# Kernel optimization log

Hardware: AMD Instinct MI355X
Metric: run time of the kernel (lower is better)

## Reference

```python
import jax, jax.numpy as jnp
import numpy as np

B, S, NC, ND, V = 16, 512, 10000, 10000, 128


def _rn(k, shape, scale=0.05):
    return jax.random.normal(k, shape, dtype=jnp.float32) * scale


def setup_inputs() -> dict:
    key = jax.random.key(0)
    ks = jax.random.split(key, 24)
    inp = {
        'c_seq': jax.random.randint(ks[0], (B, S), 0, NC),
        'd_seq': jax.random.randint(ks[1], (B, S), 0, ND),
        'r_seq': jax.random.uniform(ks[2], (B, S), dtype=jnp.float32),
        # embeddings / vectors
        'D1_w': _rn(ks[3], (ND, 1)),
        'D2_w': _rn(ks[4], (ND, V)),
        'v_r': _rn(ks[5], (V,)),
        'v_beta': _rn(ks[6], (V,)),
        # GRU (torch layout: gates ordered r,z,n; W_ih [3V,2V], W_hh [3V,V])
        'W_ih': _rn(ks[7], (3 * V, 2 * V)),
        'W_hh': _rn(ks[8], (3 * V, V)),
        'b_ih': jnp.zeros((3 * V,), jnp.float32),
        'b_hh': jnp.zeros((3 * V,), jnp.float32),
        # linear_1: V -> V -> V -> 1 (weights stored [in, out])
        'm1_W1': _rn(ks[9], (V, V)), 'm1_b1': jnp.zeros((V,), jnp.float32),
        'm1_W2': _rn(ks[10], (V, V)), 'm1_b2': jnp.zeros((V,), jnp.float32),
        'm1_W3': _rn(ks[11], (V, 1)), 'm1_b3': jnp.zeros((1,), jnp.float32),
        # linear_2: 3V -> V -> V -> 1
        'm2_W1': _rn(ks[12], (3 * V, V)), 'm2_b1': jnp.zeros((V,), jnp.float32),
        'm2_W2': _rn(ks[13], (V, V)), 'm2_b2': jnp.zeros((V,), jnp.float32),
        'm2_W3': _rn(ks[14], (V, 1)), 'm2_b3': jnp.zeros((1,), jnp.float32),
    }
    return inp


def _mlp(x, W1, b1, W2, b2, W3, b3):
    h = jax.nn.relu(x @ W1 + b1)
    h = jax.nn.relu(h @ W2 + b2)
    return h @ W3 + b3


def _gru_seq(x, W_ih, W_hh, b_ih, b_hh):
    # x: [B,S,2V] -> h_seq [B,S,V]; torch GRU gate order r,z,n
    xp = x @ W_ih.T + b_ih  # [B,S,3V]

    def step(h, xt):
        hp = h @ W_hh.T + b_hh
        xr, xz, xn = jnp.split(xt, 3, axis=-1)
        hr, hz, hn = jnp.split(hp, 3, axis=-1)
        r = jax.nn.sigmoid(xr + hr)
        z = jax.nn.sigmoid(xz + hz)
        n = jnp.tanh(xn + r * hn)
        h_new = (1.0 - z) * n + z * h
        return h_new, h_new

    h0 = jnp.zeros((x.shape[0], W_hh.shape[1]), x.dtype)
    _, hs = jax.lax.scan(step, h0, jnp.swapaxes(xp, 0, 1))  # [S,B,V]
    return jnp.swapaxes(hs, 0, 1)


def reference(c_seq, d_seq, r_seq, D1_w, D2_w, v_r, v_beta,
              W_ih, W_hh, b_ih, b_hh,
              m1_W1, m1_b1, m1_W2, m1_b2, m1_W3, m1_b3,
              m2_W1, m2_b1, m2_W2, m2_b2, m2_W3, m2_b3):
    v_d_seq = D2_w[d_seq]                     # [B,S,V]
    v_r_seq = r_seq[..., None] * v_r          # [B,S,V]

    h_seq = _gru_seq(jnp.concatenate([v_d_seq, v_r_seq], axis=-1),
                     W_ih, W_hh, b_ih, b_hh)  # [B,S,V]
    alpha_seq = _mlp(h_seq, m1_W1, m1_b1, m1_W2, m1_b2, m1_W3, m1_b3)[..., 0]  # [B,S]

    bidx = jnp.arange(c_seq.shape[0])

    def step(C, ins):
        c_t, vd_t, vr_t = ins                 # [B], [B,V], [B,V]
        beta_prev = C[bidx, c_t]              # gather: [B]
        v_beta_prev = beta_prev[:, None] * v_beta  # [B,V]
        new_c = _mlp(jnp.concatenate([v_beta_prev, vd_t, vr_t], axis=-1),
                     m2_W1, m2_b1, m2_W2, m2_b2, m2_W3, m2_b3)[:, 0]  # [B]
        C = C.at[bidx, c_t].set(new_c)        # scatter
        return C, (C, new_c)

    C0 = jnp.zeros((c_seq.shape[0], NC), jnp.float32)
    _, (C_seq, beta_seq) = jax.lax.scan(
        step, C0,
        (jnp.swapaxes(c_seq, 0, 1), jnp.swapaxes(v_d_seq, 0, 1), jnp.swapaxes(v_r_seq, 0, 1)))
    C_seq = jnp.swapaxes(C_seq, 0, 1)[..., None]   # [B,S,NC,1]
    beta_seq = jnp.swapaxes(beta_seq, 0, 1)        # [B,S]

    gamma_seq = D1_w[d_seq][..., 0]                # [B,S]
    return (alpha_seq, beta_seq, gamma_seq, h_seq, C_seq)
```

## Files before the change

kernel.cpp:

```cpp
#include <hip/hip_runtime.h>

#define Bq   16
#define Sq   512
#define Vq   128
#define NCq  10000

typedef __attribute__((ext_vector_type(8))) short short8v;
typedef __attribute__((ext_vector_type(4))) float f32x4;

#define OFF_XP     0u
#define OFF_PRE1   3145728u
#define OFF_WTIH   4194304u
#define OFF_WVRIH  4243456u
#define OFF_WVR1   4243840u
#define OFF_WVB    4243968u
#define OFF_PO     4244096u

__device__ __forceinline__ unsigned short f2bf(float x) {
    unsigned u = __builtin_bit_cast(unsigned, x);
    unsigned r = (u + 0x7fffu + ((u >> 16) & 1u)) >> 16;
    return (unsigned short)r;
}

__global__ __launch_bounds__(256) void k0_prep(
    const int* __restrict__ c_seq, const int* __restrict__ d_seq,
    const float* __restrict__ D1_w,
    const float* __restrict__ W_ih,
    const float* __restrict__ v_r, const float* __restrict__ v_beta,
    const float* __restrict__ m2W1,
    float* __restrict__ ws, float* __restrict__ gamma_out)
{
    const int blk = blockIdx.x, tid = threadIdx.x;

    if (blk < 128) {
        float* WTIH = ws + OFF_WTIH;
        int base = blk * 384;
        for (int i = tid; i < 384; i += 256) {
            int e = base + i;
            int k = e / 384, g = e % 384;
            WTIH[e] = W_ih[g * 256 + k];
        }
    } else if (blk == 128) {
        float* WVRIH = ws + OFF_WVRIH;
        float* WVR1  = ws + OFF_WVR1;
        float* WVB   = ws + OFF_WVB;
        for (int g = tid; g < 384; g += 256) {
            float a = 0.f;
            for (int k = 0; k < 128; ++k) a = fmaf(v_r[k], W_ih[g * 256 + 128 + k], a);
            WVRIH[g] = a;
        }
        if (tid < 128) {
            float a = 0.f, b = 0.f;
            for (int k = 0; k < 128; ++k) {
                a = fmaf(v_r[k],    m2W1[(256 + k) * 128 + tid], a);
                b = fmaf(v_beta[k], m2W1[k * 128 + tid],         b);
            }
            WVR1[tid] = a; WVB[tid] = b;
        }
    } else if (blk < 145) {
        const int b = blk - 129;
        __shared__ int cs[Sq];
        for (int i = tid; i < Sq; i += 256) cs[i] = c_seq[b * Sq + i];
        __syncthreads();
        int* PO = (int*)(ws + OFF_PO);
        for (int t = tid; t < Sq; t += 256) {
            int c = cs[t];
            int po = -1;
            for (int u = t - 1; u >= 0; --u) if (cs[u] == c) { po = u; break; }
            PO[t * 16 + b] = po;
        }
    } else {
        const int b = blk - 145;
        for (int s = tid; s < Sq; s += 256)
            gamma_out[b * Sq + s] = D1_w[d_seq[b * Sq + s]];
    }
}

__global__ __launch_bounds__(256) void k1_gemm(
    const int* __restrict__ d_seq, const float* __restrict__ D2_w,
    const float* __restrict__ m2W1,
    const float* __restrict__ b_ih, const float* __restrict__ b_hh,
    const float* __restrict__ r_seq, const float* __restrict__ m2b1,
    float* __restrict__ ws)
{
    __shared__ float As[64 * 128];
    __shared__ float Bs[128 * 64];
    const int blk = blockIdx.x, tid = threadIdx.x;
    const int nc = blk & 7;
    const int m0 = (blk >> 3) * 64;
    const float* WTIH = ws + OFF_WTIH;

    const float4* D2v = (const float4*)D2_w;
    for (int e = tid; e < 2048; e += 256) {
        int r = e >> 5, q = e & 31;
        int d = d_seq[m0 + r];
        *(float4*)&As[r * 128 + 4 * q] = D2v[d * 32 + q];
    }
    for (int e = tid; e < 2048; e += 256) {
        int k = e >> 4, q = e & 15;
        float4 v;
        if (nc < 6) v = *(const float4*)&WTIH[k * 384 + nc * 64 + 4 * q];
        else        v = *(const float4*)&m2W1[(128 + k) * 128 + (nc - 6) * 64 + 4 * q];
        *(float4*)&Bs[k * 64 + 4 * q] = v;
    }
    __syncthreads();

    const int tx = tid & 15, ty = tid >> 4;
    const int c0 = 4 * tx, r0 = 4 * ty;
    float acc[4][4];
#pragma unroll
    for (int i = 0; i < 4; ++i)
#pragma unroll
        for (int j = 0; j < 4; ++j) acc[i][j] = 0.f;

    for (int k = 0; k < 128; ++k) {
        float4 bv = *(const float4*)&Bs[k * 64 + c0];
#pragma unroll
        for (int i = 0; i < 4; ++i) {
            float a = As[(r0 + i) * 128 + k];
            acc[i][0] = fmaf(a, bv.x, acc[i][0]);
            acc[i][1] = fmaf(a, bv.y, acc[i][1]);
            acc[i][2] = fmaf(a, bv.z, acc[i][2]);
            acc[i][3] = fmaf(a, bv.w, acc[i][3]);
        }
    }

    float rsv[4];
#pragma unroll
    for (int i = 0; i < 4; ++i) rsv[i] = r_seq[m0 + r0 + i];

    if (nc < 6) {
        const int grow0 = nc * 64 + c0;
        float4 bi  = *(const float4*)&b_ih[grow0];
        float4 wv4 = *(const float4*)&(ws + OFF_WVRIH)[grow0];
        float4 bh4 = make_float4(0.f, 0.f, 0.f, 0.f);
        if (nc < 4) bh4 = *(const float4*)&b_hh[grow0];
        float* XP4 = ws + OFF_XP;
        const int r4 = grow0 >> 2;
#pragma unroll
        for (int i = 0; i < 4; ++i) {
            int row = m0 + r0 + i;
            int t = row & 511, bb = row >> 9;
            float4 v;
            v.x = acc[i][0] + bi.x + bh4.x + rsv[i] * wv4.x;
            v.y = acc[i][1] + bi.y + bh4.y + rsv[i] * wv4.y;
            v.z = acc[i][2] + bi.z + bh4.z + rsv[i] * wv4.z;
            v.w = acc[i][3] + bi.w + bh4.w + rsv[i] * wv4.w;
            *(float4*)&XP4[((t * 96 + r4) * 16 + bb) * 4] = v;
        }
    } else {
        const int j0 = (nc - 6) * 64 + c0;
        float4 b1v = *(const float4*)&m2b1[j0];
        float4 wr1 = *(const float4*)&(ws + OFF_WVR1)[j0];
        float* PRE1 = ws + OFF_PRE1;
#pragma unroll
        for (int i = 0; i < 4; ++i) {
            int row = m0 + r0 + i;
            float4 v;
            v.x = acc[i][0] + b1v.x + rsv[i] * wr1.x;
            v.y = acc[i][1] + b1v.y + rsv[i] * wr1.y;
            v.z = acc[i][2] + b1v.z + rsv[i] * wr1.z;
            v.w = acc[i][3] + b1v.w + rsv[i] * wr1.w;
            *(float4*)&PRE1[(size_t)row * 128 + j0] = v;
        }
    }
}

#define PLN 136
#define PLSZ (16*PLN+8)

__global__ __launch_bounds__(512, 1) void k2_scan(
    const float* __restrict__ W_hh, const float* __restrict__ b_hh,
    const float* __restrict__ m2W2, const float* __restrict__ m2b2,
    const float* __restrict__ m2W3, const float* __restrict__ m2b3,
    float* __restrict__ ws,
    float* __restrict__ hseq_out, float* __restrict__ beta_out)
{
    __shared__ __align__(16) unsigned char smem[70416];
    const int tid = threadIdx.x;
    const int l = tid & 63, wv = tid >> 6;
    const int qq = l >> 4, cb = l & 15;

    if (blockIdx.x == 0) {
        unsigned short* hP = (unsigned short*)smem;
        short8v aH[3][4];
#pragma unroll
        for (int g = 0; g < 3; ++g) {
            const float* wrow = W_hh + (g * 128 + 16 * wv + cb) * 128;
#pragma unroll
            for (int kf = 0; kf < 4; ++kf) {
                short8v hi;
#pragma unroll
                for (int e = 0; e < 8; ++e) hi[e] = (short)f2bf(wrow[kf * 32 + qq * 8 + e]);
                aH[g][kf] = hi;
            }
        }
        float bhn[4];
        *(float4*)bhn = *(const float4*)&b_hh[256 + 16 * wv + 4 * qq];
        const float* XP4 = ws + OFF_XP;

        f32x4 pxA[3], pxB[3], pxC[3];
#pragma unroll
        for (int g = 0; g < 3; ++g) {
            const int r4 = 32 * g + 4 * wv + qq;
            pxA[g] = *(const f32x4*)&XP4[((0 * 96 + r4) * 16 + cb) * 4];
            pxB[g] = *(const f32x4*)&XP4[((1 * 96 + r4) * 16 + cb) * 4];
            pxC[g] = (f32x4){0.f, 0.f, 0.f, 0.f};
        }
        float hold[4] = {0.f, 0.f, 0.f, 0.f};
        for (int i = tid; i < 2 * PLSZ; i += 512) hP[i] = 0;
        __syncthreads();

        for (int t = 0; t < 512; ++t) {
            const unsigned short* HI = hP + (t & 1) * PLSZ;
            unsigned short* HIn = hP + ((t + 1) & 1) * PLSZ;
            if (t < 510) {
#pragma unroll
                for (int g = 0; g < 3; ++g) {
                    const int r4 = 32 * g + 4 * wv + qq;
                    pxC[g] = *(const f32x4*)&XP4[(((t + 2) * 96 + r4) * 16 + cb) * 4];
                }
            }
            f32x4 C0 = {0.f,0.f,0.f,0.f}, C1 = {0.f,0.f,0.f,0.f}, C2 = {0.f,0.f,0.f,0.f};
#pragma unroll
            for (int kf = 0; kf < 4; ++kf) {
                short8v Bh = *(const short8v*)(HI + cb * PLN + kf * 32 + qq * 8);
                C0 = __builtin_amdgcn_mfma_f32_16x16x32_bf16(aH[0][kf], Bh, C0, 0, 0, 0);
                C1 = __builtin_amdgcn_mfma_f32_16x16x32_bf16(aH[1][kf], Bh, C1, 0, 0, 0);
                C2 = __builtin_amdgcn_mfma_f32_16x16x32_bf16(aH[2][kf], Bh, C2, 0, 0, 0);
            }
            float hnew[4];
#pragma unroll
            for (int i = 0; i < 4; ++i) {
                float pr = C0[i] + pxA[0][i];
                float pz = C1[i] + pxA[1][i];
                float r = 1.f / (1.f + __expf(-pr));
                float z = 1.f / (1.f + __expf(-pz));
                float hn = C2[i] + bhn[i];
                float npre = fmaf(r, hn, pxA[2][i]);
                float ax = fabsf(npre);
                float e2 = __expf(-2.f * ax);
                float n = copysignf((1.f - e2) / (1.f + e2), npre);
                float hv = (1.f - z) * n + z * hold[i];
                hold[i] = hv;
                hnew[i] = hv;
            }
            *(float4*)&hseq_out[(size_t)(cb * 512 + t) * 128 + 16 * wv + 4 * qq] =
                make_float4(hnew[0], hnew[1], hnew[2], hnew[3]);
            {
                unsigned short h0 = f2bf(hnew[0]), h1 = f2bf(hnew[1]);
                unsigned short h2 = f2bf(hnew[2]), h3 = f2bf(hnew[3]);
                uint2 hw;
                hw.x = (unsigned)h0 | ((unsigned)h1 << 16);
                hw.y = (unsigned)h2 | ((unsigned)h3 << 16);
                *(uint2*)(HIn + cb * PLN + 16 * wv + 4 * qq) = hw;
            }
#pragma unroll
            for (int g = 0; g < 3; ++g) { pxA[g] = pxB[g]; pxB[g] = pxC[g]; }
            __syncthreads();
        }
    } else {
        float* bhL = (float*)smem;
        int* poT = (int*)(smem + 32768);
        unsigned short* h1P = (unsigned short*)(smem + 65536);
        float* redL = (float*)(smem + 69904);

        {
            const int* POg = (const int*)(ws + OFF_PO);
            for (int i = tid; i < 8192; i += 512) poT[i] = POg[i];
        }
        short8v aH[4];
#pragma unroll
        for (int kf = 0; kf < 4; ++kf) {
            short8v hi;
#pragma unroll
            for (int e = 0; e < 8; ++e)
                hi[e] = (short)f2bf(m2W2[(kf * 32 + qq * 8 + e) * 128 + 16 * wv + cb]);
            aH[kf] = hi;
        }
        float w3C[4], b2C[4];
        *(float4*)w3C = *(const float4*)&m2W3[16 * wv + 4 * qq];
        *(float4*)b2C = *(const float4*)&m2b2[16 * wv + 4 * qq];
        const float b3v = m2b3[0];

        const int bb2 = tid & 15, j4 = tid >> 4;
        float wvb[4];
        *(float4*)wvb = *(const float4*)&(ws + OFF_WVB)[j4 * 4];
        const float* p1base = ws + OFF_PRE1 + (size_t)(bb2 * 512) * 128 + j4 * 4;
        f32x4 p1a = *(const f32x4*)&p1base[0];
        f32x4 p1b = *(const f32x4*)&p1base[128];
        f32x4 p1c = {0.f, 0.f, 0.f, 0.f};
        float btap = 0.f;
        __syncthreads();

        for (int t = 0; t < 512; ++t) {
            if (t < 510) p1c = *(const f32x4*)&p1base[(size_t)(t + 2) * 128];
            int po = poT[t * 16 + bb2];
            float bp = (po == t - 1) ? btap : ((po >= 0) ? bhL[bb2 * 512 + po] : 0.f);
            if (t > 0 && j4 == 0) bhL[bb2 * 512 + (t - 1)] = btap;
            {
                unsigned short h0 = f2bf(fmaxf(0.f, fmaf(bp, wvb[0], p1a[0])));
                unsigned short h1 = f2bf(fmaxf(0.f, fmaf(bp, wvb[1], p1a[1])));
                unsigned short h2 = f2bf(fmaxf(0.f, fmaf(bp, wvb[2], p1a[2])));
                unsigned short h3 = f2bf(fmaxf(0.f, fmaf(bp, wvb[3], p1a[3])));
                uint2 hw;
                hw.x = (unsigned)h0 | ((unsigned)h1 << 16);
                hw.y = (unsigned)h2 | ((unsigned)h3 << 16);
                *(uint2*)(h1P + bb2 * PLN + j4 * 4) = hw;
            }
            __syncthreads();
            f32x4 C = {0.f, 0.f, 0.f, 0.f};
#pragma unroll
            for (int kf = 0; kf < 4; ++kf) {
                short8v Bh = *(const short8v*)(h1P + cb * PLN + kf * 32 + qq * 8);
                C = __builtin_amdgcn_mfma_f32_16x16x32_bf16(aH[kf], Bh, C, 0, 0, 0);
            }
            float part = 0.f;
#pragma unroll
            for (int i = 0; i < 4; ++i)
                part = fmaf(fmaxf(0.f, C[i] + b2C[i]), w3C[i], part);
            part += __shfl_xor(part, 16);
            part += __shfl_xor(part, 32);
            if (qq == 0) redL[wv * 16 + cb] = part;
            __syncthreads();
            float bta = b3v;
#pragma unroll
            for (int w = 0; w < 8; ++w) bta += redL[w * 16 + bb2];
            btap = bta;
            p1a = p1b; p1b = p1c;
        }
        if (j4 == 0) bhL[bb2 * 512 + 511] = btap;
        __syncthreads();
        for (int i = tid; i < 8192; i += 512) beta_out[i] = bhL[i];
    }
}

__global__ __launch_bounds__(256) void k2b_fill(
    const int* __restrict__ c_seq, const float* __restrict__ beta_in,
    float* __restrict__ C_out)
{
    __shared__ int   scs[Sq];
    __shared__ float sbt[Sq];
    const int bid = blockIdx.x, tid = threadIdx.x;
    const int b = bid / 40, rem = bid % 40;
    const int chunk = rem >> 2, q = rem & 3;

    for (int i = tid; i < Sq; i += 256) {
        scs[i] = c_seq[b * Sq + i];
        sbt[i] = beta_in[b * Sq + i];
    }
    __syncthreads();

    const int c0 = chunk * 1024 + tid * 4;
    if (c0 >= NCq) return;

    float cur0 = 0.f, cur1 = 0.f, cur2 = 0.f, cur3 = 0.f;
    const int tlo = q * 128, thi = tlo + 128;
    float* base = C_out + (size_t)b * Sq * NCq + c0;

    for (int t = 0; t < tlo; ++t) {
        int ct = scs[t] - c0; float bv = sbt[t];
        cur0 = (ct == 0) ? bv : cur0;
        cur1 = (ct == 1) ? bv : cur1;
        cur2 = (ct == 2) ? bv : cur2;
        cur3 = (ct == 3) ? bv : cur3;
    }
    for (int t = tlo; t < thi; ++t) {
        int ct = scs[t] - c0; float bv = sbt[t];
        cur0 = (ct == 0) ? bv : cur0;
        cur1 = (ct == 1) ? bv : cur1;
        cur2 = (ct == 2) ? bv : cur2;
        cur3 = (ct == 3) ? bv : cur3;
        *(float4*)(base + (size_t)t * NCq) = make_float4(cur0, cur1, cur2, cur3);
    }
}

__global__ __launch_bounds__(256) void k3_alpha(
    const float* __restrict__ hseq,
    const float* __restrict__ W1, const float* __restrict__ b1,
    const float* __restrict__ W2, const float* __restrict__ b2,
    const float* __restrict__ W3, const float* __restrict__ b3,
    float* __restrict__ alpha_out)
{
    __shared__ float Hs[32 * 128];
    __shared__ float T1[32 * 128];
    __shared__ float red[4][16];
    const int blk = blockIdx.x, tid = threadIdx.x;
    const int row0 = blk * 32;

    for (int e = tid; e < 1024; e += 256) {
        int r = e >> 5, q = e & 31;
        *(float4*)&Hs[r * 128 + 4 * q] =
            *(const float4*)&hseq[(size_t)(row0 + r) * 128 + 4 * q];
    }
    __syncthreads();

    const int j = tid & 127, rh = tid >> 7;
    const float b1j = b1[j], b2j = b2[j], w3j = W3[j];
    float acc[16];
#pragma unroll
    for (int r = 0; r < 16; ++r) acc[r] = b1j;
    for (int k = 0; k < 128; ++k) {
        float w = W1[k * 128 + j];
#pragma unroll
        for (int r = 0; r < 16; ++r)
            acc[r] = fmaf(Hs[(rh * 16 + r) * 128 + k], w, acc[r]);
    }
#pragma unroll
    for (int r = 0; r < 16; ++r) {
        acc[r] = fmaxf(acc[r], 0.f);
        T1[(rh * 16 + r) * 128 + j] = acc[r];
    }
    __syncthreads();
    float acc2[16];
#pragma unroll
    for (int r = 0; r < 16; ++r) acc2[r] = b2j;
    for (int k = 0; k < 128; ++k) {
        float w = W2[k * 128 + j];
#pragma unroll
        for (int r = 0; r < 16; ++r)
            acc2[r] = fmaf(T1[(rh * 16 + r) * 128 + k], w, acc2[r]);
    }
#pragma unroll
    for (int r = 0; r < 16; ++r) {
        float p = fmaxf(acc2[r], 0.f) * w3j;
#pragma unroll
        for (int off = 1; off < 64; off <<= 1) p += __shfl_xor(p, off);
        if ((tid & 63) == 0) red[tid >> 6][r] = p;
    }
    __syncthreads();
    if (tid < 32) {
        int rr = tid & 15, g = tid >> 4;
        alpha_out[row0 + g * 16 + rr] = red[2 * g][rr] + red[2 * g + 1][rr] + b3[0];
    }
}

extern "C" void kernel_launch(void* const* d_in, const int* in_sizes, int n_in,
                              void* d_out, int out_size, void* d_ws, size_t ws_size,
                              hipStream_t stream) {
    const int*   c_seq = (const int*)d_in[0];
    const int*   d_seq = (const int*)d_in[1];
    const float* r_seq = (const float*)d_in[2];
    const float* D1_w  = (const float*)d_in[3];
    const float* D2_w  = (const float*)d_in[4];
    const float* v_r   = (const float*)d_in[5];
    const float* v_b   = (const float*)d_in[6];
    const float* W_ih  = (const float*)d_in[7];
    const float* W_hh  = (const float*)d_in[8];
    const float* b_ih  = (const float*)d_in[9];
    const float* b_hh  = (const float*)d_in[10];
    const float* m1W1  = (const float*)d_in[11];
    const float* m1b1  = (const float*)d_in[12];
    const float* m1W2  = (const float*)d_in[13];
    const float* m1b2  = (const float*)d_in[14];
    const float* m1W3  = (const float*)d_in[15];
    const float* m1b3  = (const float*)d_in[16];
    const float* m2W1  = (const float*)d_in[17];
    const float* m2b1  = (const float*)d_in[18];
    const float* m2W2  = (const float*)d_in[19];
    const float* m2b2  = (const float*)d_in[20];
    const float* m2W3  = (const float*)d_in[21];
    const float* m2b3  = (const float*)d_in[22];

    float* out   = (float*)d_out;
    float* alpha = out;
    float* beta  = out + 8192;
    float* gamma = out + 16384;
    float* hseq  = out + 24576;
    float* Cseq  = out + 1073152;
    float* ws    = (float*)d_ws;

    hipLaunchKernelGGL(k0_prep, dim3(161), dim3(256), 0, stream,
                       c_seq, d_seq, D1_w, W_ih, v_r, v_b, m2W1, ws, gamma);
    hipLaunchKernelGGL(k1_gemm, dim3(1024), dim3(256), 0, stream,
                       d_seq, D2_w, m2W1, b_ih, b_hh, r_seq, m2b1, ws);
    hipLaunchKernelGGL(k2_scan, dim3(2), dim3(512), 0, stream,
                       W_hh, b_hh, m2W2, m2b2, m2W3, m2b3, ws, hseq, beta);
    hipLaunchKernelGGL(k2b_fill, dim3(640), dim3(256), 0, stream,
                       c_seq, beta, Cseq);
    hipLaunchKernelGGL(k3_alpha, dim3(256), dim3(256), 0, stream,
                       hseq, m1W1, m1b1, m1W2, m1b2, m1W3, m1b3, alpha);
}
```

Baseline: 757.2 us.

## Split recurrent scans across batch groups and stream bf16 precomputes via LDS

The GRU scan and the beta scan each move from one workgroup handling all 16 sequences to four workgroups each handling 4 sequences, for 8 blocks total. The idea is to spread the serial recurrence over more CUs and shrink each block's per-step work. Precomputed input projections are now stored as bf16 in a per-group layout and prefetched one step ahead into LDS with global_load_lds instead of register double-buffering. In exchange, MFMA tiles sized for 16 columns are now only a quarter used, and the bf16 storage lowers the precision of the gate pre-activations.

```diff
diff --git a/kernel.cpp b/kernel.cpp
--- a/kernel.cpp
+++ b/kernel.cpp
@@ -8,18 +8,31 @@
 typedef __attribute__((ext_vector_type(8))) short short8v;
 typedef __attribute__((ext_vector_type(4))) float f32x4;
 
-#define OFF_XP     0u
-#define OFF_PRE1   3145728u
-#define OFF_WTIH   4194304u
-#define OFF_WVRIH  4243456u
-#define OFF_WVR1   4243840u
-#define OFF_WVB    4243968u
-#define OFF_PO     4244096u
+#define OFF_P1B_U  3145728u
+#define OFF_WTIH   2097152u
+#define OFF_WVRIH  2146304u
+#define OFF_WVR1   2146688u
+#define OFF_WVB    2146816u
+#define OFF_PO     2146944u
+
+#define PLN 136
+#define PLSZ (16*PLN+8)
 
 __device__ __forceinline__ unsigned short f2bf(float x) {
     unsigned u = __builtin_bit_cast(unsigned, x);
     unsigned r = (u + 0x7fffu + ((u >> 16) & 1u)) >> 16;
     return (unsigned short)r;
+}
+__device__ __forceinline__ float bfhi(unsigned u) {
+    return __builtin_bit_cast(float, u << 16);
+}
+__device__ __forceinline__ float bflo(unsigned u) {
+    return __builtin_bit_cast(float, u & 0xffff0000u);
+}
+__device__ __forceinline__ void gload_lds16(const void* g, void* l) {
+    __builtin_amdgcn_global_load_lds(
+        (const __attribute__((address_space(1))) unsigned int*)g,
+        (__attribute__((address_space(3))) unsigned int*)l, 16, 0, 0);
 }
 
 __global__ __launch_bounds__(256) void k0_prep(
@@ -135,39 +148,41 @@
         float4 wv4 = *(const float4*)&(ws + OFF_WVRIH)[grow0];
         float4 bh4 = make_float4(0.f, 0.f, 0.f, 0.f);
         if (nc < 4) bh4 = *(const float4*)&b_hh[grow0];
-        float* XP4 = ws + OFF_XP;
+        unsigned short* XPB = (unsigned short*)ws;
         const int r4 = grow0 >> 2;
 #pragma unroll
         for (int i = 0; i < 4; ++i) {
             int row = m0 + r0 + i;
             int t = row & 511, bb = row >> 9;
-            float4 v;
-            v.x = acc[i][0] + bi.x + bh4.x + rsv[i] * wv4.x;
-            v.y = acc[i][1] + bi.y + bh4.y + rsv[i] * wv4.y;
-            v.z = acc[i][2] + bi.z + bh4.z + rsv[i] * wv4.z;
-            v.w = acc[i][3] + bi.w + bh4.w + rsv[i] * wv4.w;
-            *(float4*)&XP4[((t * 96 + r4) * 16 + bb) * 4] = v;
+            float vx = acc[i][0] + bi.x + bh4.x + rsv[i] * wv4.x;
+            float vy = acc[i][1] + bi.y + bh4.y + rsv[i] * wv4.y;
+            float vz = acc[i][2] + bi.z + bh4.z + rsv[i] * wv4.z;
+            float vw = acc[i][3] + bi.w + bh4.w + rsv[i] * wv4.w;
+            uint2 p;
+            p.x = (unsigned)f2bf(vx) | ((unsigned)f2bf(vy) << 16);
+            p.y = (unsigned)f2bf(vz) | ((unsigned)f2bf(vw) << 16);
+            *(uint2*)&XPB[((size_t)((bb >> 2) * 512 + t)) * 1536 + r4 * 16 + (bb & 3) * 4] = p;
         }
     } else {
         const int j0 = (nc - 6) * 64 + c0;
         float4 b1v = *(const float4*)&m2b1[j0];
         float4 wr1 = *(const float4*)&(ws + OFF_WVR1)[j0];
-        float* PRE1 = ws + OFF_PRE1;
+        unsigned short* P1B = (unsigned short*)ws + OFF_P1B_U;
 #pragma unroll
         for (int i = 0; i < 4; ++i) {
             int row = m0 + r0 + i;
-            float4 v;
-            v.x = acc[i][0] + b1v.x + rsv[i] * wr1.x;
-            v.y = acc[i][1] + b1v.y + rsv[i] * wr1.y;
-            v.z = acc[i][2] + b1v.z + rsv[i] * wr1.z;
-            v.w = acc[i][3] + b1v.w + rsv[i] * wr1.w;
-            *(float4*)&PRE1[(size_t)row * 128 + j0] = v;
-        }
-    }
-}
-
-#define PLN 136
-#define PLSZ (16*PLN+8)
+            int t = row & 511, bb = row >> 9;
+            float vx = acc[i][0] + b1v.x + rsv[i] * wr1.x;
+            float vy = acc[i][1] + b1v.y + rsv[i] * wr1.y;
+            float vz = acc[i][2] + b1v.z + rsv[i] * wr1.z;
+            float vw = acc[i][3] + b1v.w + rsv[i] * wr1.w;
+            uint2 p;
+            p.x = (unsigned)f2bf(vx) | ((unsigned)f2bf(vy) << 16);
+            p.y = (unsigned)f2bf(vz) | ((unsigned)f2bf(vw) << 16);
+            *(uint2*)&P1B[((size_t)(t * 16 + bb)) * 128 + j0] = p;
+        }
+    }
+}
 
 __global__ __launch_bounds__(512, 1) void k2_scan(
     const float* __restrict__ W_hh, const float* __restrict__ b_hh,
@@ -176,13 +191,17 @@
     float* __restrict__ ws,
     float* __restrict__ hseq_out, float* __restrict__ beta_out)
 {
-    __shared__ __align__(16) unsigned char smem[70416];
+    __shared__ __align__(16) unsigned char smem[23040];
     const int tid = threadIdx.x;
     const int l = tid & 63, wv = tid >> 6;
     const int qq = l >> 4, cb = l & 15;
-
-    if (blockIdx.x == 0) {
-        unsigned short* hP = (unsigned short*)smem;
+    const int bgid = blockIdx.x;
+
+    if (bgid < 4) {
+        unsigned short* hP  = (unsigned short*)smem;
+        unsigned short* xps = (unsigned short*)(smem + 4 * PLSZ);
+        const unsigned short* XPB = (const unsigned short*)ws;
+
         short8v aH[3][4];
 #pragma unroll
         for (int g = 0; g < 3; ++g) {
@@ -197,30 +216,32 @@
         }
         float bhn[4];
         *(float4*)bhn = *(const float4*)&b_hh[256 + 16 * wv + 4 * qq];
-        const float* XP4 = ws + OFF_XP;
-
-        f32x4 pxA[3], pxB[3], pxC[3];
-#pragma unroll
-        for (int g = 0; g < 3; ++g) {
-            const int r4 = 32 * g + 4 * wv + qq;
-            pxA[g] = *(const f32x4*)&XP4[((0 * 96 + r4) * 16 + cb) * 4];
-            pxB[g] = *(const f32x4*)&XP4[((1 * 96 + r4) * 16 + cb) * 4];
-            pxC[g] = (f32x4){0.f, 0.f, 0.f, 0.f};
-        }
         float hold[4] = {0.f, 0.f, 0.f, 0.f};
+
         for (int i = tid; i < 2 * PLSZ; i += 512) hP[i] = 0;
+        if (wv < 3) {
+            const unsigned short* src = XPB + ((size_t)(bgid * 512)) * 1536 + wv * 512 + l * 8;
+            gload_lds16(src, xps + wv * 512);
+        }
         __syncthreads();
 
         for (int t = 0; t < 512; ++t) {
+            if (t < 511 && wv < 3) {
+                const unsigned short* src =
+                    XPB + ((size_t)(bgid * 512 + t + 1)) * 1536 + wv * 512 + l * 8;
+                gload_lds16(src, xps + ((t + 1) & 1) * 1536 + wv * 512);
+            }
+            const unsigned short* xcur = xps + (t & 1) * 1536;
+            f32x4 px[3];
+#pragma unroll
+            for (int g = 0; g < 3; ++g) {
+                uint2 u = *(const uint2*)(xcur + (32 * g + 4 * wv + qq) * 16 + (cb & 3) * 4);
+                px[g][0] = bfhi(u.x); px[g][1] = bflo(u.x);
+                px[g][2] = bfhi(u.y); px[g][3] = bflo(u.y);
+            }
             const unsigned short* HI = hP + (t & 1) * PLSZ;
             unsigned short* HIn = hP + ((t + 1) & 1) * PLSZ;
-            if (t < 510) {
-#pragma unroll
-                for (int g = 0; g < 3; ++g) {
-                    const int r4 = 32 * g + 4 * wv + qq;
-                    pxC[g] = *(const f32x4*)&XP4[(((t + 2) * 96 + r4) * 16 + cb) * 4];
-                }
-            }
+
             f32x4 C0 = {0.f,0.f,0.f,0.f}, C1 = {0.f,0.f,0.f,0.f}, C2 = {0.f,0.f,0.f,0.f};
 #pragma unroll
             for (int kf = 0; kf < 4; ++kf) {
@@ -232,12 +253,12 @@
             float hnew[4];
 #pragma unroll
             for (int i = 0; i < 4; ++i) {
-                float pr = C0[i] + pxA[0][i];
-                float pz = C1[i] + pxA[1][i];
+                float pr = C0[i] + px[0][i];
+                float pz = C1[i] + px[1][i];
                 float r = 1.f / (1.f + __expf(-pr));
                 float z = 1.f / (1.f + __expf(-pz));
                 float hn = C2[i] + bhn[i];
-                float npre = fmaf(r, hn, pxA[2][i]);
+                float npre = fmaf(r, hn, px[2][i]);
                 float ax = fabsf(npre);
                 float e2 = __expf(-2.f * ax);
                 float n = copysignf((1.f - e2) / (1.f + e2), npre);
@@ -245,9 +266,9 @@
                 hold[i] = hv;
                 hnew[i] = hv;
             }
-            *(float4*)&hseq_out[(size_t)(cb * 512 + t) * 128 + 16 * wv + 4 * qq] =
-                make_float4(hnew[0], hnew[1], hnew[2], hnew[3]);
-            {
+            if (cb < 4) {
+                *(float4*)&hseq_out[((size_t)((bgid * 4 + cb) * 512 + t)) * 128 + 16 * wv + 4 * qq] =
+                    make_float4(hnew[0], hnew[1], hnew[2], hnew[3]);
                 unsigned short h0 = f2bf(hnew[0]), h1 = f2bf(hnew[1]);
                 unsigned short h2 = f2bf(hnew[2]), h3 = f2bf(hnew[3]);
                 uint2 hw;
@@ -255,20 +276,26 @@
                 hw.y = (unsigned)h2 | ((unsigned)h3 << 16);
                 *(uint2*)(HIn + cb * PLN + 16 * wv + 4 * qq) = hw;
             }
-#pragma unroll
-            for (int g = 0; g < 3; ++g) { pxA[g] = pxB[g]; pxB[g] = pxC[g]; }
             __syncthreads();
         }
     } else {
+        const int bq = bgid - 4;
         float* bhL = (float*)smem;
-        int* poT = (int*)(smem + 32768);
-        unsigned short* h1P = (unsigned short*)(smem + 65536);
-        float* redL = (float*)(smem + 69904);
+        int*   poT = (int*)(smem + 8192);
+        unsigned short* h1P  = (unsigned short*)(smem + 16384);
+        unsigned short* xpre = (unsigned short*)(smem + 20752);
+        float* redL = (float*)(smem + 22800);
+        const unsigned short* P1B = (const unsigned short*)ws + OFF_P1B_U;
 
         {
             const int* POg = (const int*)(ws + OFF_PO);
-            for (int i = tid; i < 8192; i += 512) poT[i] = POg[i];
-        }
+            for (int i = tid; i < 2048; i += 512)
+                poT[i] = POg[(i >> 2) * 16 + 4 * bq + (i & 3)];
+        }
+        for (int i = tid; i < PLSZ; i += 512) h1P[i] = 0;
+        if (wv == 0)
+            gload_lds16(P1B + ((size_t)(4 * bq)) * 128 + l * 8, xpre);
+
         short8v aH[4];
 #pragma unroll
         for (int kf = 0; kf < 4; ++kf) {
@@ -283,32 +310,34 @@
         *(float4*)b2C = *(const float4*)&m2b2[16 * wv + 4 * qq];
         const float b3v = m2b3[0];
 
-        const int bb2 = tid & 15, j4 = tid >> 4;
-        float wvb[4];
-        *(float4*)wvb = *(const float4*)&(ws + OFF_WVB)[j4 * 4];
-        const float* p1base = ws + OFF_PRE1 + (size_t)(bb2 * 512) * 128 + j4 * 4;
-        f32x4 p1a = *(const f32x4*)&p1base[0];
-        f32x4 p1b = *(const f32x4*)&p1base[128];
-        f32x4 p1c = {0.f, 0.f, 0.f, 0.f};
+        const int bb2 = tid & 3, j4 = (tid >> 2) & 31;
+        const bool pa = tid < 128;
+        float wvb[4] = {0.f, 0.f, 0.f, 0.f};
+        if (pa) *(float4*)wvb = *(const float4*)&(ws + OFF_WVB)[j4 * 4];
         float btap = 0.f;
         __syncthreads();
 
         for (int t = 0; t < 512; ++t) {
-            if (t < 510) p1c = *(const f32x4*)&p1base[(size_t)(t + 2) * 128];
-            int po = poT[t * 16 + bb2];
-            float bp = (po == t - 1) ? btap : ((po >= 0) ? bhL[bb2 * 512 + po] : 0.f);
-            if (t > 0 && j4 == 0) bhL[bb2 * 512 + (t - 1)] = btap;
-            {
-                unsigned short h0 = f2bf(fmaxf(0.f, fmaf(bp, wvb[0], p1a[0])));
-                unsigned short h1 = f2bf(fmaxf(0.f, fmaf(bp, wvb[1], p1a[1])));
-                unsigned short h2 = f2bf(fmaxf(0.f, fmaf(bp, wvb[2], p1a[2])));
-                unsigned short h3 = f2bf(fmaxf(0.f, fmaf(bp, wvb[3], p1a[3])));
+            if (pa) {
+                int po = poT[t * 4 + bb2];
+                float bp = (po == t - 1) ? btap : ((po >= 0) ? bhL[bb2 * 512 + po] : 0.f);
+                uint2 u = *(const uint2*)(xpre + (t & 1) * 512 + bb2 * 128 + j4 * 4);
+                float h0 = fmaxf(0.f, fmaf(bp, wvb[0], bfhi(u.x)));
+                float h1 = fmaxf(0.f, fmaf(bp, wvb[1], bflo(u.x)));
+                float h2 = fmaxf(0.f, fmaf(bp, wvb[2], bfhi(u.y)));
+                float h3 = fmaxf(0.f, fmaf(bp, wvb[3], bflo(u.y)));
                 uint2 hw;
-                hw.x = (unsigned)h0 | ((unsigned)h1 << 16);
-                hw.y = (unsigned)h2 | ((unsigned)h3 << 16);
+                hw.x = (unsigned)f2bf(h0) | ((unsigned)f2bf(h1) << 16);
+                hw.y = (unsigned)f2bf(h2) | ((unsigned)f2bf(h3) << 16);
                 *(uint2*)(h1P + bb2 * PLN + j4 * 4) = hw;
             }
+            if (tid < 4 && t > 0) bhL[tid * 512 + (t - 1)] = btap;
             __syncthreads();
+
+            if (t < 511 && wv == 0)
+                gload_lds16(P1B + ((size_t)((t + 1) * 16 + 4 * bq)) * 128 + l * 8,
+                            xpre + ((t + 1) & 1) * 512);
+
             f32x4 C = {0.f, 0.f, 0.f, 0.f};
 #pragma unroll
             for (int kf = 0; kf < 4; ++kf) {
@@ -321,17 +350,18 @@
                 part = fmaf(fmaxf(0.f, C[i] + b2C[i]), w3C[i], part);
             part += __shfl_xor(part, 16);
             part += __shfl_xor(part, 32);
-            if (qq == 0) redL[wv * 16 + cb] = part;
+            if (qq == 0 && cb < 4) redL[wv * 4 + cb] = part;
             __syncthreads();
+
             float bta = b3v;
 #pragma unroll
-            for (int w = 0; w < 8; ++w) bta += redL[w * 16 + bb2];
+            for (int w = 0; w < 8; ++w) bta += redL[w * 4 + (tid & 3)];
             btap = bta;
-            p1a = p1b; p1b = p1c;
-        }
-        if (j4 == 0) bhL[bb2 * 512 + 511] = btap;
+        }
+        if (tid < 4) bhL[tid * 512 + 511] = btap;
         __syncthreads();
-        for (int i = tid; i < 8192; i += 512) beta_out[i] = bhL[i];
+        for (int i = tid; i < 2048; i += 512)
+            beta_out[(4 * bq + (i >> 9)) * 512 + (i & 511)] = bhL[i];
     }
 }
 
@@ -474,7 +504,7 @@
                        c_seq, d_seq, D1_w, W_ih, v_r, v_b, m2W1, ws, gamma);
     hipLaunchKernelGGL(k1_gemm, dim3(1024), dim3(256), 0, stream,
                        d_seq, D2_w, m2W1, b_ih, b_hh, r_seq, m2b1, ws);
-    hipLaunchKernelGGL(k2_scan, dim3(2), dim3(512), 0, stream,
+    hipLaunchKernelGGL(k2_scan, dim3(8), dim3(512), 0, stream,
                        W_hh, b_hh, m2W2, m2b2, m2W3, m2b3, ws, hseq, beta);
     hipLaunchKernelGGL(k2b_fill, dim3(640), dim3(256), 0, stream,
                        c_seq, beta, Cseq);
```

After: 750.7 us. About the same (-0.9%).
